# Optimization experiments

Measured on AMD Instinct MI355X. Metric: run time of the kernel, lower is better.

Reference implementation:

```python
import jax, jax.numpy as jnp
import numpy as np

V, D, DI, N, DTR, DC, R = 50280, 768, 1536, 16, 48, 4, 8
NLAYER, NTOP, NBASE, MAXLOOPS, L = 24, 18, 6, 10, 256
LORA_SCALE = 2.0  # alpha/rank = (rank*2)/rank
EPS = 1e-5
ALLOWED_CORE = np.array([0, 50276, 329, 378, 330, 399])  # stand-in for eos/<THINK>/' A B C D'


def rmsnorm(x, w):
    return x * jax.lax.rsqrt(jnp.mean(x * x, -1, keepdims=True) + EPS) * w


def causal_conv1d(x, w, b):
    # x: [b,l,d], w: [d,dc], b: [d]; depthwise causal conv
    xp = jnp.pad(x, ((0, 0), (DC - 1, 0), (0, 0))).transpose(0, 2, 1)  # [b,d,l+dc-1]
    y = jax.lax.conv_general_dilated(xp, w[:, None, :], (1,), 'VALID',
                                     dimension_numbers=('NCH', 'OIH', 'NCH'),
                                     feature_group_count=DI)
    return y.transpose(0, 2, 1) + b


def selective_scan(u, delta, A, B, C, Dp):
    # u,delta: [b,l,d]; A: [d,n]; B,C: [b,l,n]; Dp: [d]
    dA = jnp.exp(delta[..., None] * A)                       # [b,l,d,n]
    dBu = delta[..., None] * B[:, :, None, :] * u[..., None]  # [b,l,d,n]

    def step(h, t):
        dA_t, dBu_t, C_t = t
        h = dA_t * h + dBu_t
        return h, jnp.einsum('bdn,bn->bd', h, C_t)

    h0 = jnp.zeros((u.shape[0], DI, N), u.dtype)
    _, ys = jax.lax.scan(step, h0, (dA.swapaxes(0, 1), dBu.swapaxes(0, 1), C.swapaxes(0, 1)))
    return ys.swapaxes(0, 1) + u * Dp


def mixer(h, in_w, conv_w, conv_b, xproj_w, dt_w, dt_b, A_log, Dp, out_w, lora=None):
    if lora is not None:  # LoRALinear: W = base + scale * (B @ A)
        inA, inB, outA, outB = lora
        in_w = in_w + LORA_SCALE * (inB @ inA)
        out_w = out_w + LORA_SCALE * (outB @ outA)
    xz = h @ in_w.T                       # [b,l,2*DI]
    x, z = jnp.split(xz, 2, -1)
    x = jax.nn.silu(causal_conv1d(x, conv_w, conv_b))
    xd = x @ xproj_w.T                    # [b,l,DTR+2N]
    dt, B, C = xd[..., :DTR], xd[..., DTR:DTR + N], xd[..., DTR + N:]
    delta = jax.nn.softplus(dt @ dt_w.T + dt_b)
    y = selective_scan(x, delta, -jnp.exp(A_log), B, C, Dp)
    y = y * jax.nn.silu(z)
    return y @ out_w.T


def block(x, residual, i, P, lora=None):
    # Mamba Block: residual += x; h = norm(residual); h = mixer(h)
    residual = x if residual is None else x + residual
    h = rmsnorm(residual, P['norm_w'][i])
    h = mixer(h, P['in_proj_w'][i], P['conv_w'][i], P['conv_b'][i], P['x_proj_w'][i],
              P['dt_proj_w'][i], P['dt_proj_b'][i], P['A_log'][i], P['D_ssm'][i],
              P['out_proj_w'][i], lora)
    return h, residual


def _forward(P, input_ids, limit):
    x = P['embedding'][input_ids]
    residual = None
    for i in range(NBASE):
        x, residual = block(x, residual, i, P)
    base = x
    mask = jnp.full((V,), -jnp.inf, x.dtype)
    allowed = jnp.concatenate([input_ids[0], jnp.asarray(ALLOWED_CORE)])
    mask = mask.at[allowed].set(0.0)
    steps = []
    for step_i in range(limit):
        x = x + P['step_emb'][step_i]
        for j in range(NTOP):
            lora = (P['lora_in_A'][j], P['lora_in_B'][j], P['lora_out_A'][j], P['lora_out_B'][j])
            x, residual = block(x, residual, NBASE + j, P, lora)
        x = x + base
        x = rmsnorm(x, P['loop_norm_w'])
        xn = rmsnorm(x + residual, P['norm_f_w'])
        logits = xn @ P['lm_head_w'].T           # [1,l,V]
        steps.append(logits[0, -1, :] + mask)
    return jnp.stack(steps)                      # [limit, V]


def setup_inputs() -> dict:
    key = jax.random.key(0)
    ks = iter(jax.random.split(key, 32))

    def nrm(shape, sc=0.02):
        return jax.random.normal(next(ks), shape, jnp.float32) * sc

    A = jnp.tile(jnp.arange(1, N + 1, dtype=jnp.float32), (NLAYER, DI, 1))
    return dict(
        embedding=nrm((V, D)),
        norm_w=jnp.ones((NLAYER, D), jnp.float32),
        in_proj_w=nrm((NLAYER, 2 * DI, D)),
        conv_w=nrm((NLAYER, DI, DC), 0.1),
        conv_b=jnp.zeros((NLAYER, DI), jnp.float32),
        x_proj_w=nrm((NLAYER, DTR + 2 * N, DI)),
        dt_proj_w=nrm((NLAYER, DI, DTR), 0.1),
        dt_proj_b=nrm((NLAYER, DI), 0.5),
        A_log=jnp.log(A),
        D_ssm=jnp.ones((NLAYER, DI), jnp.float32),
        out_proj_w=nrm((NLAYER, D, DI)),
        lora_in_A=nrm((NTOP, R, D)),
        lora_in_B=nrm((NTOP, 2 * DI, R), 0.01),
        lora_out_A=nrm((NTOP, R, DI)),
        lora_out_B=nrm((NTOP, D, R), 0.01),
        norm_f_w=jnp.ones((D,), jnp.float32),
        lm_head_w=nrm((V, D)),
        step_emb=nrm((MAXLOOPS, D)),
        loop_norm_w=jnp.ones((D,), jnp.float32),
        input_ids=jax.random.randint(next(ks), (1, L), 0, V),
        limit=2,
    )


def reference(embedding, norm_w, in_proj_w, conv_w, conv_b, x_proj_w, dt_proj_w,
              dt_proj_b, A_log, D_ssm, out_proj_w, lora_in_A, lora_in_B, lora_out_A,
              lora_out_B, norm_f_w, lm_head_w, step_emb, loop_norm_w, input_ids, limit):
    P = dict(embedding=embedding, norm_w=norm_w, in_proj_w=in_proj_w, conv_w=conv_w,
             conv_b=conv_b, x_proj_w=x_proj_w, dt_proj_w=dt_proj_w, dt_proj_b=dt_proj_b,
             A_log=A_log, D_ssm=D_ssm, out_proj_w=out_proj_w, lora_in_A=lora_in_A,
             lora_in_B=lora_in_B, lora_out_A=lora_out_A, lora_out_B=lora_out_B,
             norm_f_w=norm_f_w, lm_head_w=lm_head_w, step_emb=step_emb,
             loop_norm_w=loop_norm_w)
    masked_logits = _forward(P, input_ids, int(limit))
    predicted = jnp.argmax(masked_logits, -1)   # per-loop predicted token ids
    return masked_logits, predicted
```

## Files before the change

### kernel.cpp

```cpp
#include <hip/hip_runtime.h>
#include <math.h>

#define V_SZ   50280
#define D_SZ   768
#define DI_SZ  1536
#define N_SZ   16
#define DTR_SZ 48
#define DC_SZ  4
#define R_SZ   8
#define L_SZ   256

#define NEG_BIG -1e30f

__device__ __forceinline__ float silu_f(float z) {
    return z / (1.0f + __expf(-z));
}

__global__ __launch_bounds__(256) void k_prep(
    const float* __restrict__ x, const float* __restrict__ stepv,
    float* __restrict__ res, const float* __restrict__ nw,
    float* __restrict__ h, const float* __restrict__ loraA,
    float* __restrict__ t8, int useRes)
{
    const int t = blockIdx.x, tid = threadIdx.x;
    const int lane = tid & 63, wid = tid >> 6;
    __shared__ float wsum[4];
    __shared__ float facs;
    __shared__ float w8[8][4];

    float v[3];
    float ss = 0.0f;
#pragma unroll
    for (int i = 0; i < 3; ++i) {
        int d = tid + 256 * i;
        float a = x[t * D_SZ + d];
        if (useRes) a += res[t * D_SZ + d];
        if (stepv)  a += stepv[d];
        v[i] = a;
        ss = fmaf(a, a, ss);
    }
#pragma unroll
    for (int off = 32; off; off >>= 1) ss += __shfl_down(ss, off);
    if (lane == 0) wsum[wid] = ss;
    __syncthreads();
    if (tid == 0)
        facs = rsqrtf((wsum[0] + wsum[1] + wsum[2] + wsum[3]) * (1.0f / 768.0f) + 1e-5f);
    __syncthreads();
    const float fac = facs;

    float hh[3];
#pragma unroll
    for (int i = 0; i < 3; ++i) {
        int d = tid + 256 * i;
        res[t * D_SZ + d] = v[i];
        hh[i] = v[i] * fac * nw[d];
        h[t * D_SZ + d] = hh[i];
    }

    if (loraA) {
        float p[8] = {};
#pragma unroll
        for (int i = 0; i < 3; ++i) {
            int d = tid + 256 * i;
#pragma unroll
            for (int r = 0; r < 8; ++r) p[r] = fmaf(hh[i], loraA[r * D_SZ + d], p[r]);
        }
#pragma unroll
        for (int r = 0; r < 8; ++r) {
            float q = p[r];
#pragma unroll
            for (int off = 32; off; off >>= 1) q += __shfl_down(q, off);
            if (lane == 0) w8[r][wid] = q;
        }
        __syncthreads();
        if (tid < 8) t8[t * 8 + tid] = w8[tid][0] + w8[tid][1] + w8[tid][2] + w8[tid][3];
    }
}

template<bool GATE, bool LORA, bool DUAL>
__global__ __launch_bounds__(256) void k_gemm(
    const float* __restrict__ A, int lda,
    const float* __restrict__ Z, int ldz,
    const float* __restrict__ W, int K,
    float* __restrict__ C, int ldc,
    float* __restrict__ C2,
    const float* __restrict__ T8,
    const float* __restrict__ LB)
{
    __shared__ __align__(16) float As[16][68];
    __shared__ __align__(16) float Bs[16][68];
    const int tid = threadIdx.x;
    const int tx = tid & 15, ty = tid >> 4;
    const int row0 = blockIdx.y * 64, col0 = blockIdx.x * 64;
    const int sr = tid >> 2;
    const int sk = (tid & 3) * 4;

    const float* Ap = A + (size_t)(row0 + sr) * lda + sk;
    const float* Zp = nullptr;
    if constexpr (GATE) Zp = Z + (size_t)(row0 + sr) * ldz + sk;
    const float* Wp = W + (size_t)(col0 + sr) * K + sk;

    float acc[4][4] = {};
    const int nkt = K / 16;

    float4 a4 = *(const float4*)(Ap);
    if constexpr (GATE) {
        float4 z4 = *(const float4*)(Zp);
        a4.x *= silu_f(z4.x); a4.y *= silu_f(z4.y);
        a4.z *= silu_f(z4.z); a4.w *= silu_f(z4.w);
    }
    float4 b4 = *(const float4*)(Wp);

    for (int kt = 0; kt < nkt; ++kt) {
        As[sk + 0][sr] = a4.x; As[sk + 1][sr] = a4.y;
        As[sk + 2][sr] = a4.z; As[sk + 3][sr] = a4.w;
        Bs[sk + 0][sr] = b4.x; Bs[sk + 1][sr] = b4.y;
        Bs[sk + 2][sr] = b4.z; Bs[sk + 3][sr] = b4.w;
        __syncthreads();
        if (kt + 1 < nkt) {
            a4 = *(const float4*)(Ap + (kt + 1) * 16);
            if constexpr (GATE) {
                float4 z4 = *(const float4*)(Zp + (kt + 1) * 16);
                a4.x *= silu_f(z4.x); a4.y *= silu_f(z4.y);
                a4.z *= silu_f(z4.z); a4.w *= silu_f(z4.w);
            }
            b4 = *(const float4*)(Wp + (kt + 1) * 16);
        }
#pragma unroll
        for (int kk = 0; kk < 16; ++kk) {
            float4 av = *(const float4*)&As[kk][ty * 4];
            float4 bv = *(const float4*)&Bs[kk][tx * 4];
            acc[0][0] = fmaf(av.x, bv.x, acc[0][0]);
            acc[0][1] = fmaf(av.x, bv.y, acc[0][1]);
            acc[0][2] = fmaf(av.x, bv.z, acc[0][2]);
            acc[0][3] = fmaf(av.x, bv.w, acc[0][3]);
            acc[1][0] = fmaf(av.y, bv.x, acc[1][0]);
            acc[1][1] = fmaf(av.y, bv.y, acc[1][1]);
            acc[1][2] = fmaf(av.y, bv.z, acc[1][2]);
            acc[1][3] = fmaf(av.y, bv.w, acc[1][3]);
            acc[2][0] = fmaf(av.z, bv.x, acc[2][0]);
            acc[2][1] = fmaf(av.z, bv.y, acc[2][1]);
            acc[2][2] = fmaf(av.z, bv.z, acc[2][2]);
            acc[2][3] = fmaf(av.z, bv.w, acc[2][3]);
            acc[3][0] = fmaf(av.w, bv.x, acc[3][0]);
            acc[3][1] = fmaf(av.w, bv.y, acc[3][1]);
            acc[3][2] = fmaf(av.w, bv.z, acc[3][2]);
            acc[3][3] = fmaf(av.w, bv.w, acc[3][3]);
        }
        __syncthreads();
    }

    if constexpr (LORA) {
#pragma unroll
        for (int i = 0; i < 4; ++i) {
            const float* t8p = T8 + (size_t)(row0 + ty * 4 + i) * 8;
#pragma unroll
            for (int j = 0; j < 4; ++j) {
                const float* lbp = LB + (size_t)(col0 + tx * 4 + j) * 8;
                float s = 0.0f;
#pragma unroll
                for (int r = 0; r < 8; ++r) s = fmaf(t8p[r], lbp[r], s);
                acc[i][j] = fmaf(2.0f, s, acc[i][j]);
            }
        }
    }

#pragma unroll
    for (int i = 0; i < 4; ++i) {
        float4 v;
        v.x = acc[i][0]; v.y = acc[i][1]; v.z = acc[i][2]; v.w = acc[i][3];
        size_t off = (size_t)(row0 + ty * 4 + i) * ldc + col0 + tx * 4;
        *(float4*)(C + off) = v;
        if constexpr (DUAL) *(float4*)(C2 + off) = v;
    }
}

__global__ __launch_bounds__(256) void k_convx(
    const float* __restrict__ xz, const float* __restrict__ cw, const float* __restrict__ cb,
    const float* __restrict__ xw, const float* __restrict__ dtw, const float* __restrict__ dtb,
    float* __restrict__ xc, float* __restrict__ Bc, float* __restrict__ Cc,
    float* __restrict__ delta)
{
    const int t = blockIdx.x, tid = threadIdx.x;
    const int lane = tid & 63, wid = tid >> 6;
    __shared__ __align__(16) float xcs[DI_SZ];
    __shared__ __align__(16) float xds[80];

#pragma unroll
    for (int c = 0; c < 6; ++c) {
        int d = tid + 256 * c;
        float a = cb[d];
#pragma unroll
        for (int k = 0; k < 4; ++k) {
            int tt = t - 3 + k;
            if (tt >= 0) a = fmaf(cw[d * 4 + k], xz[(size_t)tt * 3072 + d], a);
        }
        a = silu_f(a);
        xcs[d] = a;
        xc[(size_t)t * DI_SZ + d] = a;
    }
    __syncthreads();

    const float4* xcs4 = (const float4*)xcs;
    for (int i = wid; i < 80; i += 4) {
        const float4* w4 = (const float4*)(xw + (size_t)i * DI_SZ);
        float p = 0.0f;
#pragma unroll
        for (int j = 0; j < 6; ++j) {
            float4 xv = xcs4[lane + 64 * j];
            float4 wv = w4[lane + 64 * j];
            p += xv.x * wv.x + xv.y * wv.y + xv.z * wv.z + xv.w * wv.w;
        }
#pragma unroll
        for (int off = 32; off; off >>= 1) p += __shfl_down(p, off);
        if (lane == 0) xds[i] = p;
    }
    __syncthreads();

    if (tid < 16) {
        Bc[t * N_SZ + tid] = xds[DTR_SZ + tid];
        Cc[t * N_SZ + tid] = xds[DTR_SZ + N_SZ + tid];
    }

#pragma unroll
    for (int c = 0; c < 6; ++c) {
        int d = tid + 256 * c;
        float s = dtb[d];
        const float4* w4 = (const float4*)(dtw + (size_t)d * DTR_SZ);
#pragma unroll
        for (int i = 0; i < 12; ++i) {
            float4 wv = w4[i];
            float4 xv = *(const float4*)&xds[i * 4];
            s += wv.x * xv.x + wv.y * xv.y + wv.z * xv.z + wv.w * xv.w;
        }
        delta[(size_t)t * DI_SZ + d] = (s > 20.0f) ? s : log1pf(__expf(s));
    }
}

__global__ __launch_bounds__(256) void k_scan(
    const float* __restrict__ delta, const float* __restrict__ xc,
    const float* __restrict__ Bc, const float* __restrict__ Cc,
    const float* __restrict__ Alog, const float* __restrict__ Dp,
    float* __restrict__ y)
{
    const int gid = blockIdx.x * 256 + threadIdx.x;
    const int d = gid >> 4, n = gid & 15;
    const float a = -__expf(Alog[d * N_SZ + n]);
    const float dp = Dp[d];
    float hst = 0.0f;
    for (int t = 0; t < L_SZ; ++t) {
        float dl = delta[(size_t)t * DI_SZ + d];
        float u  = xc[(size_t)t * DI_SZ + d];
        float bv = Bc[t * N_SZ + n];
        float cv = Cc[t * N_SZ + n];
        hst = fmaf(__expf(dl * a), hst, dl * bv * u);
        float p = hst * cv;
        p += __shfl_xor(p, 1);
        p += __shfl_xor(p, 2);
        p += __shfl_xor(p, 4);
        p += __shfl_xor(p, 8);
        if (n == 0) y[(size_t)t * DI_SZ + d] = fmaf(u, dp, p);
    }
}

__global__ __launch_bounds__(256) void k_t8o(
    const float* __restrict__ y, const float* __restrict__ xz,
    const float* __restrict__ outA, float* __restrict__ t8)
{
    const int t = blockIdx.x, tid = threadIdx.x;
    const int lane = tid & 63, wid = tid >> 6;
    __shared__ float w8[8][4];
    float p[8] = {};
#pragma unroll
    for (int c = 0; c < 6; ++c) {
        int d = tid + 256 * c;
        float z = xz[(size_t)t * 3072 + DI_SZ + d];
        float yg = y[(size_t)t * DI_SZ + d] * silu_f(z);
#pragma unroll
        for (int r = 0; r < 8; ++r) p[r] = fmaf(yg, outA[r * DI_SZ + d], p[r]);
    }
#pragma unroll
    for (int r = 0; r < 8; ++r) {
        float q = p[r];
#pragma unroll
        for (int off = 32; off; off >>= 1) q += __shfl_down(q, off);
        if (lane == 0) w8[r][wid] = q;
    }
    __syncthreads();
    if (tid < 8) t8[t * 8 + tid] = w8[tid][0] + w8[tid][1] + w8[tid][2] + w8[tid][3];
}

__global__ __launch_bounds__(256) void k_loopend(
    float* __restrict__ x, const float* __restrict__ base, const float* __restrict__ res,
    const float* __restrict__ lnw, const float* __restrict__ nfw, float* __restrict__ xnl)
{
    const int t = blockIdx.x, tid = threadIdx.x;
    const int lane = tid & 63, wid = tid >> 6;
    __shared__ float wsum[4];
    __shared__ float facs;

    float v[3];
    float ss = 0.0f;
#pragma unroll
    for (int i = 0; i < 3; ++i) {
        int d = tid + 256 * i;
        v[i] = x[t * D_SZ + d] + base[t * D_SZ + d];
        ss = fmaf(v[i], v[i], ss);
    }
#pragma unroll
    for (int off = 32; off; off >>= 1) ss += __shfl_down(ss, off);
    if (lane == 0) wsum[wid] = ss;
    __syncthreads();
    if (tid == 0)
        facs = rsqrtf((wsum[0] + wsum[1] + wsum[2] + wsum[3]) * (1.0f / 768.0f) + 1e-5f);
    __syncthreads();
    float fac = facs;

    float xv[3];
#pragma unroll
    for (int i = 0; i < 3; ++i) {
        int d = tid + 256 * i;
        xv[i] = v[i] * fac * lnw[d];
        x[t * D_SZ + d] = xv[i];
    }

    if (t == L_SZ - 1) {
        float w2[3];
        float ss2 = 0.0f;
#pragma unroll
        for (int i = 0; i < 3; ++i) {
            int d = tid + 256 * i;
            w2[i] = xv[i] + res[t * D_SZ + d];
            ss2 = fmaf(w2[i], w2[i], ss2);
        }
#pragma unroll
        for (int off = 32; off; off >>= 1) ss2 += __shfl_down(ss2, off);
        __syncthreads();
        if (lane == 0) wsum[wid] = ss2;
        __syncthreads();
        if (tid == 0)
            facs = rsqrtf((wsum[0] + wsum[1] + wsum[2] + wsum[3]) * (1.0f / 768.0f) + 1e-5f);
        __syncthreads();
        float f2 = facs;
#pragma unroll
        for (int i = 0; i < 3; ++i) {
            int d = tid + 256 * i;
            xnl[d] = w2[i] * f2 * nfw[d];
        }
    }
}

__global__ __launch_bounds__(256) void k_logits(
    const float* __restrict__ xn, const float* __restrict__ lmw,
    const float* __restrict__ mask, float* __restrict__ out)
{
    const int tid = threadIdx.x, lane = tid & 63, wid = tid >> 6;
    const int v = blockIdx.x * 4 + wid;
    const float4* x4 = (const float4*)xn;
    const float4* w4 = (const float4*)(lmw + (size_t)v * D_SZ);
    float p = 0.0f;
#pragma unroll
    for (int i = 0; i < 3; ++i) {
        float4 a = x4[lane + 64 * i];
        float4 b = w4[lane + 64 * i];
        p += a.x * b.x + a.y * b.y + a.z * b.z + a.w * b.w;
    }
#pragma unroll
    for (int off = 32; off; off >>= 1) p += __shfl_down(p, off);
    if (lane == 0) out[v] = p + mask[v];
}

__global__ __launch_bounds__(256) void k_argmax(
    const float* __restrict__ lg, float* __restrict__ outp)
{
    const int tid = threadIdx.x;
    float best = -__builtin_inff();
    int bi = 0x7fffffff;
    for (int v = tid; v < V_SZ; v += 256) {
        float val = lg[v];
        if (val > best) { best = val; bi = v; }
    }
    __shared__ float sv[256];
    __shared__ int si[256];
    sv[tid] = best; si[tid] = bi;
    __syncthreads();
    for (int s = 128; s; s >>= 1) {
        if (tid < s) {
            if (sv[tid + s] > sv[tid] ||
                (sv[tid + s] == sv[tid] && si[tid + s] < si[tid])) {
                sv[tid] = sv[tid + s]; si[tid] = si[tid + s];
            }
        }
        __syncthreads();
    }
    if (tid == 0) outp[0] = (float)si[0];
}

__global__ void k_maskfill(float* __restrict__ mask)
{
    int i = blockIdx.x * 256 + threadIdx.x;
    if (i < V_SZ) mask[i] = NEG_BIG;
}

__global__ void k_maskset(const int* __restrict__ ids, float* __restrict__ mask)
{
    int tid = threadIdx.x;
    if (tid < 256) {
        mask[ids[tid]] = 0.0f;
    } else if (tid < 262) {
        const int core[6] = {0, 50276, 329, 378, 330, 399};
        mask[core[tid - 256]] = 0.0f;
    }
}

__global__ __launch_bounds__(256) void k_embed(
    const float* __restrict__ emb, const int* __restrict__ ids, float* __restrict__ x)
{
    int t = blockIdx.x, tid = threadIdx.x;
    int id = ids[t];
#pragma unroll
    for (int i = 0; i < 3; ++i)
        x[(size_t)t * D_SZ + tid + 256 * i] = emb[(size_t)id * D_SZ + tid + 256 * i];
}

extern "C" void kernel_launch(void* const* d_in, const int* in_sizes, int n_in,
                              void* d_out, int out_size, void* d_ws, size_t ws_size,
                              hipStream_t stream)
{
    (void)in_sizes; (void)n_in; (void)ws_size;

    const float* emb   = (const float*)d_in[0];
    const float* normw = (const float*)d_in[1];
    const float* inw   = (const float*)d_in[2];
    const float* convw = (const float*)d_in[3];
    const float* convb = (const float*)d_in[4];
    const float* xpw   = (const float*)d_in[5];
    const float* dtw   = (const float*)d_in[6];
    const float* dtb   = (const float*)d_in[7];
    const float* alog  = (const float*)d_in[8];
    const float* dssm  = (const float*)d_in[9];
    const float* outw  = (const float*)d_in[10];
    const float* liA   = (const float*)d_in[11];
    const float* liB   = (const float*)d_in[12];
    const float* loA   = (const float*)d_in[13];
    const float* loB   = (const float*)d_in[14];
    const float* nfw   = (const float*)d_in[15];
    const float* lmw   = (const float*)d_in[16];
    const float* stepe = (const float*)d_in[17];
    const float* lnw   = (const float*)d_in[18];
    const int*   ids   = (const int*)d_in[19];
    float* out = (float*)d_out;
    const int limit = out_size / (V_SZ + 1);

    float* p = (float*)d_ws;
    float* x    = p; p += 256 * 768;
    float* res  = p; p += 256 * 768;
    float* base = p; p += 256 * 768;
    float* h    = p; p += 256 * 768;
    float* xz   = p; p += 256 * 3072;
    float* xcb  = p; p += 256 * 1536;
    float* dlt  = p; p += 256 * 1536;
    float* yb   = p; p += 256 * 1536;
    float* Bc   = p; p += 256 * 16;
    float* Cc   = p; p += 256 * 16;
    float* tA   = p; p += 256 * 8;
    float* tO   = p; p += 256 * 8;
    float* xnl  = p; p += 768;
    float* mask = p; p += V_SZ;

    k_maskfill<<<(V_SZ + 255) / 256, 256, 0, stream>>>(mask);
    k_maskset<<<1, 320, 0, stream>>>(ids, mask);
    k_embed<<<L_SZ, 256, 0, stream>>>(emb, ids, x);

    auto run_block = [&](int li, int j, const float* stepv, int useRes, bool dual) {
        k_prep<<<L_SZ, 256, 0, stream>>>(
            x, stepv, res, normw + (size_t)li * D_SZ, h,
            j >= 0 ? liA + (size_t)j * R_SZ * D_SZ : nullptr, tA, useRes);

        dim3 gA(3072 / 64, 4), gD(768 / 64, 4);
        const float* W1 = inw + (size_t)li * 3072 * 768;
        if (j >= 0)
            k_gemm<false, true, false><<<gA, 256, 0, stream>>>(
                h, 768, nullptr, 0, W1, 768, xz, 3072, nullptr,
                tA, liB + (size_t)j * 3072 * R_SZ);
        else
            k_gemm<false, false, false><<<gA, 256, 0, stream>>>(
                h, 768, nullptr, 0, W1, 768, xz, 3072, nullptr, nullptr, nullptr);

        k_convx<<<L_SZ, 256, 0, stream>>>(
            xz, convw + (size_t)li * DI_SZ * DC_SZ, convb + (size_t)li * DI_SZ,
            xpw + (size_t)li * 80 * DI_SZ, dtw + (size_t)li * DI_SZ * DTR_SZ,
            dtb + (size_t)li * DI_SZ, xcb, Bc, Cc, dlt);

        k_scan<<<DI_SZ * N_SZ / 256, 256, 0, stream>>>(
            dlt, xcb, Bc, Cc, alog + (size_t)li * DI_SZ * N_SZ,
            dssm + (size_t)li * DI_SZ, yb);

        const float* W2 = outw + (size_t)li * 768 * 1536;
        if (j >= 0) {
            k_t8o<<<L_SZ, 256, 0, stream>>>(yb, xz, loA + (size_t)j * R_SZ * DI_SZ, tO);
            k_gemm<true, true, false><<<gD, 256, 0, stream>>>(
                yb, 1536, xz + 1536, 3072, W2, 1536, x, 768, nullptr,
                tO, loB + (size_t)j * 768 * R_SZ);
        } else if (dual) {
            k_gemm<true, false, true><<<gD, 256, 0, stream>>>(
                yb, 1536, xz + 1536, 3072, W2, 1536, x, 768, base, nullptr, nullptr);
        } else {
            k_gemm<true, false, false><<<gD, 256, 0, stream>>>(
                yb, 1536, xz + 1536, 3072, W2, 1536, x, 768, nullptr, nullptr, nullptr);
        }
    };

    for (int li = 0; li < 6; ++li)
        run_block(li, -1, nullptr, li > 0 ? 1 : 0, li == 5);

    for (int s = 0; s < limit; ++s) {
        for (int jj = 0; jj < 18; ++jj)
            run_block(6 + jj, jj, jj == 0 ? stepe + (size_t)s * D_SZ : nullptr, 1, false);
        k_loopend<<<L_SZ, 256, 0, stream>>>(x, base, res, lnw, nfw, xnl);
        k_logits<<<V_SZ / 4, 256, 0, stream>>>(xnl, lmw, mask, out + (size_t)s * V_SZ);
        k_argmax<<<1, 256, 0, stream>>>(out + (size_t)s * V_SZ,
                                        out + (size_t)limit * V_SZ + s);
    }
}
```

Measured before the change: 12.31 ms.

## Split-K GEMMs with partial buffers reduced in consumers, wider tiles, fused gating

Both projection GEMMs now use split-K over blockIdx.z (4 splits for in_proj, 8 for out_proj). Each split writes its own partial-sum buffer, and the next kernel (prep, convx, loopend) adds the partials together. The GEMM tile grows to 128 rows with 8x8 or 8x4 outputs per thread. The silu(z) gate moves out of the GEMM A-load into convx and the scan epilogue, and the scan prefetches the next timestep's inputs. The aim is to fill more of the GPU, since the small M=256 GEMMs launched few blocks. In exchange, the consumer kernels must read extra partial buffers, which adds memory traffic.

```diff
diff --git a/kernel.cpp b/kernel.cpp
--- a/kernel.cpp
+++ b/kernel.cpp
@@ -10,6 +10,11 @@
 #define R_SZ   8
 #define L_SZ   256
 
+#define NSA 4
+#define NSD 8
+#define PSX (256 * 768)
+#define PSZ (256 * 3072)
+
 #define NEG_BIG -1e30f
 
 __device__ __forceinline__ float silu_f(float z) {
@@ -17,10 +22,10 @@
 }
 
 __global__ __launch_bounds__(256) void k_prep(
-    const float* __restrict__ x, const float* __restrict__ stepv,
+    const float* __restrict__ xp, int nsum, const float* __restrict__ stepv,
     float* __restrict__ res, const float* __restrict__ nw,
     float* __restrict__ h, const float* __restrict__ loraA,
-    float* __restrict__ t8, int useRes)
+    float* __restrict__ t8, int useRes, float* __restrict__ baseOut)
 {
     const int t = blockIdx.x, tid = threadIdx.x;
     const int lane = tid & 63, wid = tid >> 6;
@@ -33,8 +38,10 @@
 #pragma unroll
     for (int i = 0; i < 3; ++i) {
         int d = tid + 256 * i;
-        float a = x[t * D_SZ + d];
-        if (useRes) a += res[t * D_SZ + d];
+        float a = xp[(size_t)t * D_SZ + d];
+        for (int q = 1; q < nsum; ++q) a += xp[(size_t)q * PSX + (size_t)t * D_SZ + d];
+        if (baseOut) baseOut[(size_t)t * D_SZ + d] = a;
+        if (useRes) a += res[(size_t)t * D_SZ + d];
         if (stepv)  a += stepv[d];
         v[i] = a;
         ss = fmaf(a, a, ss);
@@ -52,9 +59,9 @@
 #pragma unroll
     for (int i = 0; i < 3; ++i) {
         int d = tid + 256 * i;
-        res[t * D_SZ + d] = v[i];
+        res[(size_t)t * D_SZ + d] = v[i];
         hh[i] = v[i] * fac * nw[d];
-        h[t * D_SZ + d] = hh[i];
+        h[(size_t)t * D_SZ + d] = hh[i];
     }
 
     if (loraA) {
@@ -77,108 +84,127 @@
     }
 }
 
-template<bool GATE, bool LORA, bool DUAL>
+template<bool LORA, bool WIDE>
 __global__ __launch_bounds__(256) void k_gemm(
     const float* __restrict__ A, int lda,
-    const float* __restrict__ Z, int ldz,
-    const float* __restrict__ W, int K,
-    float* __restrict__ C, int ldc,
-    float* __restrict__ C2,
-    const float* __restrict__ T8,
-    const float* __restrict__ LB)
-{
-    __shared__ __align__(16) float As[16][68];
-    __shared__ __align__(16) float Bs[16][68];
+    const float* __restrict__ W, int ldw,
+    int kChunk, float* __restrict__ Cp, int ldc,
+    const float* __restrict__ T8, const float* __restrict__ LB)
+{
+    constexpr int TN = WIDE ? 8 : 4;
+    constexpr int BN = WIDE ? 128 : 64;
+    __shared__ __align__(16) float As[16][132];
+    __shared__ __align__(16) float Bs[16][WIDE ? 140 : 68];
+
     const int tid = threadIdx.x;
+    const int col0 = blockIdx.x * BN, row0 = blockIdx.y * 128;
+    const int kBase = blockIdx.z * kChunk;
+    const int nkt = kChunk >> 4;
+
+    const int ar = tid >> 1, ak = (tid & 1) << 3;
+    const float* Ap = A + (size_t)(row0 + ar) * lda + kBase + ak;
+
+    const int bc = WIDE ? (tid >> 1) : (tid >> 2);
+    const int bk = WIDE ? ((tid & 1) << 3) : ((tid & 3) << 2);
+    const float* Wp = W + (size_t)(col0 + bc) * ldw + kBase + bk;
+    const int bcs = WIDE ? (bc + ((bc >> 5) << 2)) : bc;
+
+    float4 a0 = *(const float4*)Ap;
+    float4 a1 = *(const float4*)(Ap + 4);
+    float4 b0 = *(const float4*)Wp;
+    float4 b1 = {};
+    if constexpr (WIDE) b1 = *(const float4*)(Wp + 4);
+
     const int tx = tid & 15, ty = tid >> 4;
-    const int row0 = blockIdx.y * 64, col0 = blockIdx.x * 64;
-    const int sr = tid >> 2;
-    const int sk = (tid & 3) * 4;
-
-    const float* Ap = A + (size_t)(row0 + sr) * lda + sk;
-    const float* Zp = nullptr;
-    if constexpr (GATE) Zp = Z + (size_t)(row0 + sr) * ldz + sk;
-    const float* Wp = W + (size_t)(col0 + sr) * K + sk;
-
-    float acc[4][4] = {};
-    const int nkt = K / 16;
-
-    float4 a4 = *(const float4*)(Ap);
-    if constexpr (GATE) {
-        float4 z4 = *(const float4*)(Zp);
-        a4.x *= silu_f(z4.x); a4.y *= silu_f(z4.y);
-        a4.z *= silu_f(z4.z); a4.w *= silu_f(z4.w);
-    }
-    float4 b4 = *(const float4*)(Wp);
+    const int crow = ty * 8;
+    const int ccol = tx * TN;
+    const int cswz = WIDE ? (ccol + ((ccol >> 5) << 2)) : ccol;
+
+    float acc[8][TN];
+#pragma unroll
+    for (int i = 0; i < 8; ++i)
+#pragma unroll
+        for (int j = 0; j < TN; ++j) acc[i][j] = 0.0f;
 
     for (int kt = 0; kt < nkt; ++kt) {
-        As[sk + 0][sr] = a4.x; As[sk + 1][sr] = a4.y;
-        As[sk + 2][sr] = a4.z; As[sk + 3][sr] = a4.w;
-        Bs[sk + 0][sr] = b4.x; Bs[sk + 1][sr] = b4.y;
-        Bs[sk + 2][sr] = b4.z; Bs[sk + 3][sr] = b4.w;
+        As[ak + 0][ar] = a0.x; As[ak + 1][ar] = a0.y;
+        As[ak + 2][ar] = a0.z; As[ak + 3][ar] = a0.w;
+        As[ak + 4][ar] = a1.x; As[ak + 5][ar] = a1.y;
+        As[ak + 6][ar] = a1.z; As[ak + 7][ar] = a1.w;
+        Bs[bk + 0][bcs] = b0.x; Bs[bk + 1][bcs] = b0.y;
+        Bs[bk + 2][bcs] = b0.z; Bs[bk + 3][bcs] = b0.w;
+        if constexpr (WIDE) {
+            Bs[bk + 4][bcs] = b1.x; Bs[bk + 5][bcs] = b1.y;
+            Bs[bk + 6][bcs] = b1.z; Bs[bk + 7][bcs] = b1.w;
+        }
         __syncthreads();
         if (kt + 1 < nkt) {
-            a4 = *(const float4*)(Ap + (kt + 1) * 16);
-            if constexpr (GATE) {
-                float4 z4 = *(const float4*)(Zp + (kt + 1) * 16);
-                a4.x *= silu_f(z4.x); a4.y *= silu_f(z4.y);
-                a4.z *= silu_f(z4.z); a4.w *= silu_f(z4.w);
+            a0 = *(const float4*)(Ap + (kt + 1) * 16);
+            a1 = *(const float4*)(Ap + (kt + 1) * 16 + 4);
+            b0 = *(const float4*)(Wp + (kt + 1) * 16);
+            if constexpr (WIDE) b1 = *(const float4*)(Wp + (kt + 1) * 16 + 4);
+        }
+#pragma unroll
+        for (int kk = 0; kk < 16; ++kk) {
+            float4 av0 = *(const float4*)&As[kk][crow];
+            float4 av1 = *(const float4*)&As[kk][crow + 4];
+            float4 bv0 = *(const float4*)&Bs[kk][cswz];
+            float a_[8] = {av0.x, av0.y, av0.z, av0.w, av1.x, av1.y, av1.z, av1.w};
+            if constexpr (WIDE) {
+                float4 bv1 = *(const float4*)&Bs[kk][cswz + 4];
+                float b_[8] = {bv0.x, bv0.y, bv0.z, bv0.w, bv1.x, bv1.y, bv1.z, bv1.w};
+#pragma unroll
+                for (int i = 0; i < 8; ++i)
+#pragma unroll
+                    for (int j = 0; j < 8; ++j)
+                        acc[i][j] = fmaf(a_[i], b_[j], acc[i][j]);
+            } else {
+                float b_[4] = {bv0.x, bv0.y, bv0.z, bv0.w};
+#pragma unroll
+                for (int i = 0; i < 8; ++i)
+#pragma unroll
+                    for (int j = 0; j < 4; ++j)
+                        acc[i][j] = fmaf(a_[i], b_[j], acc[i][j]);
             }
-            b4 = *(const float4*)(Wp + (kt + 1) * 16);
-        }
-#pragma unroll
-        for (int kk = 0; kk < 16; ++kk) {
-            float4 av = *(const float4*)&As[kk][ty * 4];
-            float4 bv = *(const float4*)&Bs[kk][tx * 4];
-            acc[0][0] = fmaf(av.x, bv.x, acc[0][0]);
-            acc[0][1] = fmaf(av.x, bv.y, acc[0][1]);
-            acc[0][2] = fmaf(av.x, bv.z, acc[0][2]);
-            acc[0][3] = fmaf(av.x, bv.w, acc[0][3]);
-            acc[1][0] = fmaf(av.y, bv.x, acc[1][0]);
-            acc[1][1] = fmaf(av.y, bv.y, acc[1][1]);
-            acc[1][2] = fmaf(av.y, bv.z, acc[1][2]);
-            acc[1][3] = fmaf(av.y, bv.w, acc[1][3]);
-            acc[2][0] = fmaf(av.z, bv.x, acc[2][0]);
-            acc[2][1] = fmaf(av.z, bv.y, acc[2][1]);
-            acc[2][2] = fmaf(av.z, bv.z, acc[2][2]);
-            acc[2][3] = fmaf(av.z, bv.w, acc[2][3]);
-            acc[3][0] = fmaf(av.w, bv.x, acc[3][0]);
-            acc[3][1] = fmaf(av.w, bv.y, acc[3][1]);
-            acc[3][2] = fmaf(av.w, bv.z, acc[3][2]);
-            acc[3][3] = fmaf(av.w, bv.w, acc[3][3]);
         }
         __syncthreads();
     }
 
     if constexpr (LORA) {
-#pragma unroll
-        for (int i = 0; i < 4; ++i) {
-            const float* t8p = T8 + (size_t)(row0 + ty * 4 + i) * 8;
-#pragma unroll
-            for (int j = 0; j < 4; ++j) {
-                const float* lbp = LB + (size_t)(col0 + tx * 4 + j) * 8;
-                float s = 0.0f;
-#pragma unroll
-                for (int r = 0; r < 8; ++r) s = fmaf(t8p[r], lbp[r], s);
-                acc[i][j] = fmaf(2.0f, s, acc[i][j]);
+        if (blockIdx.z == 0) {
+#pragma unroll
+            for (int i = 0; i < 8; ++i) {
+                const float* t8p = T8 + (size_t)(row0 + crow + i) * 8;
+#pragma unroll
+                for (int j = 0; j < TN; ++j) {
+                    const float* lbp = LB + (size_t)(col0 + ccol + j) * 8;
+                    float s = 0.0f;
+#pragma unroll
+                    for (int r = 0; r < 8; ++r) s = fmaf(t8p[r], lbp[r], s);
+                    acc[i][j] = fmaf(2.0f, s, acc[i][j]);
+                }
             }
         }
     }
 
-#pragma unroll
-    for (int i = 0; i < 4; ++i) {
-        float4 v;
-        v.x = acc[i][0]; v.y = acc[i][1]; v.z = acc[i][2]; v.w = acc[i][3];
-        size_t off = (size_t)(row0 + ty * 4 + i) * ldc + col0 + tx * 4;
-        *(float4*)(C + off) = v;
-        if constexpr (DUAL) *(float4*)(C2 + off) = v;
+    float* Co = Cp + (size_t)blockIdx.z * 256 * ldc;
+#pragma unroll
+    for (int i = 0; i < 8; ++i) {
+        size_t off = (size_t)(row0 + crow + i) * ldc + col0 + ccol;
+        float4 v0; v0.x = acc[i][0]; v0.y = acc[i][1]; v0.z = acc[i][2]; v0.w = acc[i][3];
+        *(float4*)(Co + off) = v0;
+        if constexpr (WIDE) {
+            float4 v1; v1.x = acc[i][4]; v1.y = acc[i][5]; v1.z = acc[i][6]; v1.w = acc[i][7];
+            *(float4*)(Co + off + 4) = v1;
+        }
     }
 }
 
 __global__ __launch_bounds__(256) void k_convx(
-    const float* __restrict__ xz, const float* __restrict__ cw, const float* __restrict__ cb,
+    const float* __restrict__ xzp, const float* __restrict__ cw, const float* __restrict__ cb,
     const float* __restrict__ xw, const float* __restrict__ dtw, const float* __restrict__ dtb,
-    float* __restrict__ xc, float* __restrict__ Bc, float* __restrict__ Cc,
+    float* __restrict__ xc, float* __restrict__ gg,
+    float* __restrict__ Bc, float* __restrict__ Cc,
     float* __restrict__ delta)
 {
     const int t = blockIdx.x, tid = threadIdx.x;
@@ -193,11 +219,23 @@
 #pragma unroll
         for (int k = 0; k < 4; ++k) {
             int tt = t - 3 + k;
-            if (tt >= 0) a = fmaf(cw[d * 4 + k], xz[(size_t)tt * 3072 + d], a);
+            if (tt >= 0) {
+                float xv = xzp[(size_t)tt * 3072 + d];
+#pragma unroll
+                for (int q = 1; q < NSA; ++q)
+                    xv += xzp[(size_t)q * PSZ + (size_t)tt * 3072 + d];
+                a = fmaf(cw[d * 4 + k], xv, a);
+            }
         }
         a = silu_f(a);
         xcs[d] = a;
         xc[(size_t)t * DI_SZ + d] = a;
+
+        float z = xzp[(size_t)t * 3072 + DI_SZ + d];
+#pragma unroll
+        for (int q = 1; q < NSA; ++q)
+            z += xzp[(size_t)q * PSZ + (size_t)t * 3072 + DI_SZ + d];
+        gg[(size_t)t * DI_SZ + d] = silu_f(z);
     }
     __syncthreads();
 
@@ -241,31 +279,33 @@
     const float* __restrict__ delta, const float* __restrict__ xc,
     const float* __restrict__ Bc, const float* __restrict__ Cc,
     const float* __restrict__ Alog, const float* __restrict__ Dp,
-    float* __restrict__ y)
+    const float* __restrict__ gg, float* __restrict__ y)
 {
     const int gid = blockIdx.x * 256 + threadIdx.x;
     const int d = gid >> 4, n = gid & 15;
     const float a = -__expf(Alog[d * N_SZ + n]);
     const float dp = Dp[d];
     float hst = 0.0f;
+    float dl = delta[d], u = xc[d], bv = Bc[n], cv = Cc[n];
     for (int t = 0; t < L_SZ; ++t) {
-        float dl = delta[(size_t)t * DI_SZ + d];
-        float u  = xc[(size_t)t * DI_SZ + d];
-        float bv = Bc[t * N_SZ + n];
-        float cv = Cc[t * N_SZ + n];
+        const int tn = (t + 1 < L_SZ) ? t + 1 : t;
+        float dl2 = delta[(size_t)tn * DI_SZ + d];
+        float u2  = xc[(size_t)tn * DI_SZ + d];
+        float bv2 = Bc[tn * N_SZ + n];
+        float cv2 = Cc[tn * N_SZ + n];
         hst = fmaf(__expf(dl * a), hst, dl * bv * u);
         float p = hst * cv;
         p += __shfl_xor(p, 1);
         p += __shfl_xor(p, 2);
         p += __shfl_xor(p, 4);
         p += __shfl_xor(p, 8);
-        if (n == 0) y[(size_t)t * DI_SZ + d] = fmaf(u, dp, p);
+        if (n == 0) y[(size_t)t * DI_SZ + d] = fmaf(u, dp, p) * gg[(size_t)t * DI_SZ + d];
+        dl = dl2; u = u2; bv = bv2; cv = cv2;
     }
 }
 
 __global__ __launch_bounds__(256) void k_t8o(
-    const float* __restrict__ y, const float* __restrict__ xz,
-    const float* __restrict__ outA, float* __restrict__ t8)
+    const float* __restrict__ y, const float* __restrict__ outA, float* __restrict__ t8)
 {
     const int t = blockIdx.x, tid = threadIdx.x;
     const int lane = tid & 63, wid = tid >> 6;
@@ -274,8 +314,7 @@
 #pragma unroll
     for (int c = 0; c < 6; ++c) {
         int d = tid + 256 * c;
-        float z = xz[(size_t)t * 3072 + DI_SZ + d];
-        float yg = y[(size_t)t * DI_SZ + d] * silu_f(z);
+        float yg = y[(size_t)t * DI_SZ + d];
 #pragma unroll
         for (int r = 0; r < 8; ++r) p[r] = fmaf(yg, outA[r * DI_SZ + d], p[r]);
     }
@@ -291,7 +330,8 @@
 }
 
 __global__ __launch_bounds__(256) void k_loopend(
-    float* __restrict__ x, const float* __restrict__ base, const float* __restrict__ res,
+    float* __restrict__ xp, int nsum, const float* __restrict__ base,
+    const float* __restrict__ res,
     const float* __restrict__ lnw, const float* __restrict__ nfw, float* __restrict__ xnl)
 {
     const int t = blockIdx.x, tid = threadIdx.x;
@@ -304,8 +344,10 @@
 #pragma unroll
     for (int i = 0; i < 3; ++i) {
         int d = tid + 256 * i;
-        v[i] = x[t * D_SZ + d] + base[t * D_SZ + d];
-        ss = fmaf(v[i], v[i], ss);
+        float a = base[(size_t)t * D_SZ + d];
+        for (int q = 0; q < nsum; ++q) a += xp[(size_t)q * PSX + (size_t)t * D_SZ + d];
+        v[i] = a;
+        ss = fmaf(a, a, ss);
     }
 #pragma unroll
     for (int off = 32; off; off >>= 1) ss += __shfl_down(ss, off);
@@ -321,7 +363,7 @@
     for (int i = 0; i < 3; ++i) {
         int d = tid + 256 * i;
         xv[i] = v[i] * fac * lnw[d];
-        x[t * D_SZ + d] = xv[i];
+        xp[(size_t)t * D_SZ + d] = xv[i];
     }
 
     if (t == L_SZ - 1) {
@@ -330,7 +372,7 @@
 #pragma unroll
         for (int i = 0; i < 3; ++i) {
             int d = tid + 256 * i;
-            w2[i] = xv[i] + res[t * D_SZ + d];
+            w2[i] = xv[i] + res[(size_t)t * D_SZ + d];
             ss2 = fmaf(w2[i], w2[i], ss2);
         }
 #pragma unroll
@@ -453,11 +495,12 @@
     const int limit = out_size / (V_SZ + 1);
 
     float* p = (float*)d_ws;
-    float* x    = p; p += 256 * 768;
+    float* xp   = p; p += NSD * PSX;
     float* res  = p; p += 256 * 768;
     float* base = p; p += 256 * 768;
     float* h    = p; p += 256 * 768;
-    float* xz   = p; p += 256 * 3072;
+    float* xzp  = p; p += NSA * PSZ;
+    float* gg   = p; p += 256 * 1536;
     float* xcb  = p; p += 256 * 1536;
     float* dlt  = p; p += 256 * 1536;
     float* yb   = p; p += 256 * 1536;
@@ -470,54 +513,58 @@
 
     k_maskfill<<<(V_SZ + 255) / 256, 256, 0, stream>>>(mask);
     k_maskset<<<1, 320, 0, stream>>>(ids, mask);
-    k_embed<<<L_SZ, 256, 0, stream>>>(emb, ids, x);
-
-    auto run_block = [&](int li, int j, const float* stepv, int useRes, bool dual) {
+    k_embed<<<L_SZ, 256, 0, stream>>>(emb, ids, xp);
+
+    auto run_block = [&](int li, int j, const float* stepv, int useRes,
+                         float* baseOut, int nsumIn) {
         k_prep<<<L_SZ, 256, 0, stream>>>(
-            x, stepv, res, normw + (size_t)li * D_SZ, h,
-            j >= 0 ? liA + (size_t)j * R_SZ * D_SZ : nullptr, tA, useRes);
-
-        dim3 gA(3072 / 64, 4), gD(768 / 64, 4);
+            xp, nsumIn, stepv, res, normw + (size_t)li * D_SZ, h,
+            j >= 0 ? liA + (size_t)j * R_SZ * D_SZ : nullptr, tA, useRes, baseOut);
+
+        dim3 gA(3072 / 128, 2, NSA);
         const float* W1 = inw + (size_t)li * 3072 * 768;
         if (j >= 0)
-            k_gemm<false, true, false><<<gA, 256, 0, stream>>>(
-                h, 768, nullptr, 0, W1, 768, xz, 3072, nullptr,
+            k_gemm<true, true><<<gA, 256, 0, stream>>>(
+                h, 768, W1, 768, 768 / NSA, xzp, 3072,
                 tA, liB + (size_t)j * 3072 * R_SZ);
         else
-            k_gemm<false, false, false><<<gA, 256, 0, stream>>>(
-                h, 768, nullptr, 0, W1, 768, xz, 3072, nullptr, nullptr, nullptr);
+            k_gemm<false, true><<<gA, 256, 0, stream>>>(
+                h, 768, W1, 768, 768 / NSA, xzp, 3072, nullptr, nullptr);
 
         k_convx<<<L_SZ, 256, 0, stream>>>(
-            xz, convw + (size_t)li * DI_SZ * DC_SZ, convb + (size_t)li * DI_SZ,
+            xzp, convw + (size_t)li * DI_SZ * DC_SZ, convb + (size_t)li * DI_SZ,
             xpw + (size_t)li * 80 * DI_SZ, dtw + (size_t)li * DI_SZ * DTR_SZ,
-            dtb + (size_t)li * DI_SZ, xcb, Bc, Cc, dlt);
+            dtb + (size_t)li * DI_SZ, xcb, gg, Bc, Cc, dlt);
 
         k_scan<<<DI_SZ * N_SZ / 256, 256, 0, stream>>>(
             dlt, xcb, Bc, Cc, alog + (size_t)li * DI_SZ * N_SZ,
-            dssm + (size_t)li * DI_SZ, yb);
-
+            dssm + (size_t)li * DI_SZ, gg, yb);
+
+        dim3 gD(768 / 64, 2, NSD);
         const float* W2 = outw + (size_t)li * 768 * 1536;
         if (j >= 0) {
-            k_t8o<<<L_SZ, 256, 0, stream>>>(yb, xz, loA + (size_t)j * R_SZ * DI_SZ, tO);
-            k_gemm<true, true, false><<<gD, 256, 0, stream>>>(
-                yb, 1536, xz + 1536, 3072, W2, 1536, x, 768, nullptr,
+            k_t8o<<<L_SZ, 256, 0, stream>>>(yb, loA + (size_t)j * R_SZ * DI_SZ, tO);
+            k_gemm<true, false><<<gD, 256, 0, stream>>>(
+                yb, 1536, W2, 1536, 1536 / NSD, xp, 768,
                 tO, loB + (size_t)j * 768 * R_SZ);
-        } else if (dual) {
-            k_gemm<true, false, true><<<gD, 256, 0, stream>>>(
-                yb, 1536, xz + 1536, 3072, W2, 1536, x, 768, base, nullptr, nullptr);
         } else {
-            k_gemm<true, false, false><<<gD, 256, 0, stream>>>(
-                yb, 1536, xz + 1536, 3072, W2, 1536, x, 768, nullptr, nullptr, nullptr);
+            k_gemm<false, false><<<gD, 256, 0, stream>>>(
+                yb, 1536, W2, 1536, 1536 / NSD, xp, 768, nullptr, nullptr);
         }
     };
 
-    for (int li = 0; li < 6; ++li)
-        run_block(li, -1, nullptr, li > 0 ? 1 : 0, li == 5);
+    run_block(0, -1, nullptr, 0, nullptr, 1);
+    for (int li = 1; li < 6; ++li)
+        run_block(li, -1, nullptr, 1, nullptr, NSD);
 
     for (int s = 0; s < limit; ++s) {
-        for (int jj = 0; jj < 18; ++jj)
-            run_block(6 + jj, jj, jj == 0 ? stepe + (size_t)s * D_SZ : nullptr, 1, false);
-        k_loopend<<<L_SZ, 256, 0, stream>>>(x, base, res, lnw, nfw, xnl);
+        for (int jj = 0; jj < 18; ++jj) {
+            run_block(6 + jj, jj,
+                      jj == 0 ? stepe + (size_t)s * D_SZ : nullptr, 1,
+                      (jj == 0 && s == 0) ? base : nullptr,
+                      (jj == 0 && s > 0) ? 1 : NSD);
+        }
+        k_loopend<<<L_SZ, 256, 0, stream>>>(xp, NSD, base, res, lnw, nfw, xnl);
         k_logits<<<V_SZ / 4, 256, 0, stream>>>(xnl, lmw, mask, out + (size_t)s * V_SZ);
         k_argmax<<<1, 256, 0, stream>>>(out + (size_t)s * V_SZ,
                                         out + (size_t)limit * V_SZ + s);
```

After: 10.04 ms. -18.4%, faster.
